# Performance work log

Measured on AMD Instinct MI355X. Metric: run time of the kernel, lower is better.

The kernel has to match this reference:

```python
import jax, jax.numpy as jnp
import numpy as np

B, N, D, L, NREPEAT = 32, 577, 384, 12, 4
H = 4 * D  # mlp hidden
EPS = 1e-6


def ln(x, w, b):
    mu = jnp.mean(x, axis=-1, keepdims=True)
    var = jnp.mean(jnp.square(x - mu), axis=-1, keepdims=True)
    return (x - mu) * jax.lax.rsqrt(var + EPS) * w + b


def setup_inputs() -> dict:
    key = jax.random.key(0)
    ks = jax.random.split(key, 16)
    s = 0.02
    return {
        "x": jax.random.normal(ks[0], (B, N, D), dtype=jnp.float32),
        "norm1_w": jnp.ones((L, D), jnp.float32),
        "norm1_b": jnp.zeros((L, D), jnp.float32),
        "qkv_w": jax.random.normal(ks[1], (L, 3 * D, D), jnp.float32) * s,
        "qkv_b": jnp.zeros((L, 3 * D), jnp.float32),
        "qn_w": jnp.ones((L, D), jnp.float32),
        "qn_b": jnp.zeros((L, D), jnp.float32),
        "kn_w": jnp.ones((L, D), jnp.float32),
        "kn_b": jnp.zeros((L, D), jnp.float32),
        "an_w": jnp.ones((L, D), jnp.float32),
        "an_b": jnp.zeros((L, D), jnp.float32),
        "proj_w": jax.random.normal(ks[2], (L, D, D), jnp.float32) * s,
        "proj_b": jnp.zeros((L, D), jnp.float32),
        "ls1": jnp.full((L, D), 1e-5, jnp.float32),
        "norm2_w": jnp.ones((L, D), jnp.float32),
        "norm2_b": jnp.zeros((L, D), jnp.float32),
        "fc1_w": jax.random.normal(ks[3], (L, H, D), jnp.float32) * s,
        "fc1_b": jnp.zeros((L, H), jnp.float32),
        "fc2_w": jax.random.normal(ks[4], (L, D, H), jnp.float32) * s,
        "fc2_b": jnp.zeros((L, D), jnp.float32),
        "ls2": jnp.full((L, D), 1e-5, jnp.float32),
    }


def _forward(x, norm1_w, norm1_b, qkv_w, qkv_b, qn_w, qn_b, kn_w, kn_b,
             an_w, an_b, proj_w, proj_b, ls1, norm2_w, norm2_b,
             fc1_w, fc1_b, fc2_w, fc2_b, ls2):
    scale = 1.0 / np.sqrt(D).astype(np.float32)
    x_prime = x
    history = []  # list of [B, 1, D] cls tokens, grows each repeat
    for _ in range(NREPEAT):
        new_cls = x[:, 0:1]
        x = jnp.concatenate([new_cls, x_prime[:, 1:]], axis=1)  # [B, N, D]
        mem = jnp.concatenate([x] + history, axis=1)            # [B, N+t, D]
        for l in range(L):
            res1 = x
            xn = ln(x, norm1_w[l], norm1_b[l])
            # manual qkv split: q from normed x, k/v from UNNORMED mem
            q = xn @ qkv_w[l, :D].T + qkv_b[l, :D]
            k = mem @ qkv_w[l, D:2 * D].T + qkv_b[l, D:2 * D]
            v = mem @ qkv_w[l, 2 * D:].T + qkv_b[l, 2 * D:]
            q = ln(q, qn_w[l], qn_b[l])
            k = ln(k, kn_w[l], kn_b[l])
            # single-head SDPA over full width D
            attn = jax.nn.softmax(jnp.einsum('bqd,bkd->bqk', q, k) * scale, axis=-1)
            prod = jnp.einsum('bqk,bkd->bqd', attn, v)
            prod = ln(prod, an_w[l], an_b[l])
            proj = prod @ proj_w[l].T + proj_b[l]
            x = proj * ls1[l] + res1
            res2 = x
            x2 = ln(x, norm2_w[l], norm2_b[l])
            h = jax.nn.gelu(x2 @ fc1_w[l].T + fc1_b[l], approximate=False)
            x1 = h @ fc2_w[l].T + fc2_b[l]
            x = x1 * ls2[l] + res2
        history.append(new_cls)
    return x


def reference(x, norm1_w, norm1_b, qkv_w, qkv_b, qn_w, qn_b, kn_w, kn_b,
              an_w, an_b, proj_w, proj_b, ls1, norm2_w, norm2_b,
              fc1_w, fc1_b, fc2_w, fc2_b, ls2):
    return _forward(x, norm1_w, norm1_b, qkv_w, qkv_b, qn_w, qn_b, kn_w, kn_b,
                    an_w, an_b, proj_w, proj_b, ls1, norm2_w, norm2_b,
                    fc1_w, fc1_b, fc2_w, fc2_b, ls2)
```

## Files before the change

### kernel.cpp

```cpp
#include <hip/hip_runtime.h>
#include <math.h>

#define BB 32
#define NN 577
#define DD 384
#define HD 1536
#define LL 12
#define MP 640
#define NRPT 4

typedef __attribute__((ext_vector_type(8))) short bf16x8;
typedef __attribute__((ext_vector_type(4))) float f32x4;

__device__ __forceinline__ unsigned short f2bf(float f){
  unsigned u = __builtin_bit_cast(unsigned, f);
  u += 0x7fffu + ((u >> 16) & 1u);
  return (unsigned short)(u >> 16);
}
__device__ __forceinline__ float bf2f(unsigned short s){
  unsigned u = ((unsigned)s) << 16;
  return __builtin_bit_cast(float, u);
}

__device__ __forceinline__ void async16(void* lds, const void* g){
  __builtin_amdgcn_global_load_lds(
      (const __attribute__((address_space(1))) unsigned int*)g,
      (__attribute__((address_space(3))) unsigned int*)lds, 16, 0, 0);
}

__global__ void prep_k(float* __restrict__ x, const float* __restrict__ xp,
                       float* __restrict__ cls_r, const float* __restrict__ cls_hist,
                       unsigned short* __restrict__ mem, int r){
  int i = blockIdx.x * 256 + threadIdx.x;
  if (i >= BB*MP*DD) return;
  int d = i % DD;
  int n = (i / DD) % MP;
  int b = i / (MP*DD);
  float v;
  if (n == 0){ v = x[(size_t)b*NN*DD + d]; cls_r[b*DD + d] = v; }
  else if (n < NN){ v = xp[((size_t)b*NN + n)*DD + d]; x[((size_t)b*NN + n)*DD + d] = v; }
  else if (n < NN + r){ v = cls_hist[(size_t)(n-NN)*BB*DD + b*DD + d]; }
  else v = 0.f;
  mem[i] = f2bf(v);
}

__global__ void cast_all_k(const float* __restrict__ qkvw, const float* __restrict__ pw,
                           const float* __restrict__ f1w, const float* __restrict__ f2w,
                           unsigned short* __restrict__ wbuf){
  int i = blockIdx.x * 256 + threadIdx.x;
  const int QKV = 3*DD*DD;
  const int PRJ = DD*DD;
  const int F1  = HD*DD;
  const int TOT = QKV + PRJ + 2*F1;
  if (i >= LL*TOT) return;
  int l = i / TOT, j = i % TOT;
  float v;
  if (j < QKV) v = qkvw[(size_t)l*QKV + j];
  else if (j < QKV+PRJ) v = pw[(size_t)l*PRJ + (j-QKV)];
  else if (j < QKV+PRJ+F1) v = f1w[(size_t)l*F1 + (j-QKV-PRJ)];
  else v = f2w[(size_t)l*F1 + (j-QKV-PRJ-F1)];
  wbuf[i] = f2bf(v);
}

template<typename T>
__global__ __launch_bounds__(256) void ln4_k(const T* __restrict__ in, const float* __restrict__ w,
                                             const float* __restrict__ bias, unsigned short* __restrict__ out,
                                             int nrows){
  int row = blockIdx.x*4 + (threadIdx.x >> 6);
  if (row >= nrows) return;
  int lane = threadIdx.x & 63;
  const T* p = in + (size_t)row*DD;
  float v[6];
  if constexpr (sizeof(T) == 4){
    const float* pf = (const float*)p;
    float4 a = *(const float4*)(pf + lane*4);
    float2 c = *(const float2*)(pf + 256 + lane*2);
    v[0]=a.x; v[1]=a.y; v[2]=a.z; v[3]=a.w; v[4]=c.x; v[5]=c.y;
  } else {
    const unsigned short* ps = (const unsigned short*)p;
    ushort4 a = *(const ushort4*)(ps + lane*4);
    ushort2 c = *(const ushort2*)(ps + 256 + lane*2);
    v[0]=bf2f(a.x); v[1]=bf2f(a.y); v[2]=bf2f(a.z); v[3]=bf2f(a.w);
    v[4]=bf2f(c.x); v[5]=bf2f(c.y);
  }
  float s = v[0]+v[1]+v[2]+v[3]+v[4]+v[5];
  #pragma unroll
  for (int o=32;o;o>>=1) s += __shfl_xor(s, o, 64);
  float mu = s * (1.f/DD);
  float q = 0.f;
  #pragma unroll
  for (int i=0;i<6;i++){ float t = v[i]-mu; q += t*t; }
  #pragma unroll
  for (int o=32;o;o>>=1) q += __shfl_xor(q, o, 64);
  float rs = rsqrtf(q*(1.f/DD) + 1e-6f);
  float4 w4 = *(const float4*)(w + lane*4);
  float2 w2 = *(const float2*)(w + 256 + lane*2);
  float4 b4 = *(const float4*)(bias + lane*4);
  float2 b2 = *(const float2*)(bias + 256 + lane*2);
  unsigned short* po = out + (size_t)row*DD;
  ushort4 o4;
  o4.x = f2bf((v[0]-mu)*rs*w4.x + b4.x);
  o4.y = f2bf((v[1]-mu)*rs*w4.y + b4.y);
  o4.z = f2bf((v[2]-mu)*rs*w4.z + b4.z);
  o4.w = f2bf((v[3]-mu)*rs*w4.w + b4.w);
  *(ushort4*)(po + lane*4) = o4;
  ushort2 o2;
  o2.x = f2bf((v[4]-mu)*rs*w2.x + b2.x);
  o2.y = f2bf((v[5]-mu)*rs*w2.y + b2.y);
  *(ushort2*)(po + 256 + lane*2) = o2;
}

__global__ __launch_bounds__(256) void fixup_k(
    const unsigned short* __restrict__ mem,
    const unsigned short* __restrict__ wq,
    const float* __restrict__ qkvb,
    const float* __restrict__ knw, const float* __restrict__ knb,
    unsigned short* __restrict__ kc,
    unsigned short* __restrict__ vc,
    int row2){
  int task = blockIdx.x*4 + (threadIdx.x >> 6);
  int lane = threadIdx.x & 63;
  int kind = task & 1;
  int rsel = (task >> 1) & 1;
  int b    = task >> 2;
  int row  = rsel ? row2 : 0;
  const unsigned short* mrow = mem + ((size_t)b*MP + row)*DD;
  const unsigned short* W = wq + (size_t)(kind+1)*DD*DD;
  const float* bias = qkvb + (kind+1)*DD;

  float acc[6] = {0,0,0,0,0,0};
  for (int i=0;i<48;i++){
    bf16x8 m8 = *(const bf16x8*)(mrow + i*8);
    float mf[8];
    #pragma unroll
    for (int j=0;j<8;j++) mf[j] = bf2f((unsigned short)m8[j]);
    #pragma unroll
    for (int c=0;c<6;c++){
      bf16x8 w8 = *(const bf16x8*)(W + (size_t)(lane + c*64)*DD + i*8);
      #pragma unroll
      for (int j=0;j<8;j++) acc[c] += mf[j]*bf2f((unsigned short)w8[j]);
    }
  }
  #pragma unroll
  for (int c=0;c<6;c++) acc[c] += bias[lane + c*64];

  if (kind == 0){
    float s1 = 0.f, s2 = 0.f;
    #pragma unroll
    for (int c=0;c<6;c++){ s1 += acc[c]; s2 += acc[c]*acc[c]; }
    #pragma unroll
    for (int o=32;o;o>>=1){ s1 += __shfl_xor(s1, o, 64); s2 += __shfl_xor(s2, o, 64); }
    float mu = s1*(1.f/DD);
    float var = s2*(1.f/DD) - mu*mu;
    float rs = rsqrtf(fmaxf(var, 0.f) + 1e-6f);
    unsigned short* out = kc + ((size_t)b*MP + row)*DD;
    #pragma unroll
    for (int c=0;c<6;c++){
      int col = lane + c*64;
      out[col] = f2bf((acc[c]-mu)*rs*knw[col] + knb[col]);
    }
  } else {
    #pragma unroll
    for (int c=0;c<6;c++){
      int d = lane + c*64;
      vc[((size_t)b*DD + d)*MP + row] = f2bf(acc[c]);
    }
  }
}

template<int EPI>
__global__ __launch_bounds__(256) void gemm128(
    const unsigned short* __restrict__ A, int lda, int arows, long sA,
    const unsigned short* __restrict__ B, int ldb, int brows, long sB,
    const float* __restrict__ bias,
    int K, int N,
    float* __restrict__ outF, unsigned short* __restrict__ outB,
    int ldo, int orows, long sO,
    const float* __restrict__ ls){

  __shared__ unsigned short a_sh[2][128*32];
  __shared__ unsigned short b_sh[2][128*32];

  int tid  = threadIdx.x;
  int wave = tid >> 6, lane = tid & 63;
  int lr = lane & 15, kg = lane >> 4;
  int wm = wave >> 1, wn = wave & 1;
  int z = blockIdx.z;
  int row0 = blockIdx.y * 128;
  int col0 = blockIdx.x * 128;

  const unsigned short* Ab = A + (size_t)z*sA;
  const unsigned short* Bb = B + (size_t)z*sB;

  f32x4 zf = {0.f,0.f,0.f,0.f};
  f32x4 acc[4][4];
  #pragma unroll
  for (int i=0;i<4;i++)
    #pragma unroll
    for (int j=0;j<4;j++) acc[i][j] = zf;

  int ra[2], rb[2], kc[2];
  #pragma unroll
  for (int it=0; it<2; it++){
    int c = tid + it*256;
    int r = row0 + (c>>2); if (r > arows-1) r = arows-1;
    ra[it] = r;
    r = col0 + (c>>2); if (r > brows-1) r = brows-1;
    rb[it] = r;
    kc[it] = (c&3)*8;
  }

  for (int k0 = 0; k0 < K; k0 += 64){
    #pragma unroll
    for (int p=0;p<2;p++){
      #pragma unroll
      for (int it=0; it<2; it++){
        unsigned short* la = &a_sh[p][(it*256 + wave*64)*8];
        unsigned short* lb = &b_sh[p][(it*256 + wave*64)*8];
        async16(la, Ab + (size_t)ra[it]*lda + k0 + p*32 + kc[it]);
        async16(lb, Bb + (size_t)rb[it]*ldb + k0 + p*32 + kc[it]);
      }
    }
    __syncthreads();
    #pragma unroll
    for (int p=0;p<2;p++){
      bf16x8 af[4], bfr[4];
      #pragma unroll
      for (int i=0;i<4;i++){
        af[i]  = *(const bf16x8*)&a_sh[p][(wm*64 + i*16 + lr)*32 + kg*8];
        bfr[i] = *(const bf16x8*)&b_sh[p][(wn*64 + i*16 + lr)*32 + kg*8];
      }
      #pragma unroll
      for (int i=0;i<4;i++)
        #pragma unroll
        for (int j=0;j<4;j++)
          acc[i][j] = __builtin_amdgcn_mfma_f32_16x16x32_bf16(af[i], bfr[j], acc[i][j], 0,0,0);
    }
    __syncthreads();
  }

  float* oF = outF ? outF + (size_t)z*sO : nullptr;
  unsigned short* oB = outB ? outB + (size_t)z*sO : nullptr;

  #pragma unroll
  for (int mi=0;mi<4;mi++)
    #pragma unroll
    for (int ni=0;ni<4;ni++)
      #pragma unroll
      for (int r=0;r<4;r++){
        int row = row0 + wm*64 + mi*16 + kg*4 + r;
        int col = col0 + wn*64 + ni*16 + lr;
        if (row >= orows || col >= N) continue;
        float vv = acc[mi][ni][r];
        size_t idx = (size_t)row*ldo + col;
        if (EPI == 0){
          if (bias) vv += bias[col];
          oB[idx] = f2bf(vv);
        } else if (EPI == 1){
          vv += bias[row];
          oB[idx] = f2bf(vv);
        } else if (EPI == 2){
          vv += bias[col];
          oF[idx] = vv*ls[col] + oF[idx];
        } else {
          vv += bias[col];
          float g = 0.5f*vv*(1.f + erff(vv*0.70710678118f));
          oB[idx] = f2bf(g);
        }
      }
}

__global__ __launch_bounds__(256, 2) void attn_k(
    const unsigned short* __restrict__ qraw,
    const float* __restrict__ qw, const float* __restrict__ qb_,
    const unsigned short* __restrict__ kb,
    const unsigned short* __restrict__ vT,
    const float* __restrict__ anw, const float* __restrict__ anb,
    unsigned short* __restrict__ out, int M){

  __shared__ unsigned short k_sh[32*384];
  __shared__ unsigned short v_sh[384*32];
  __shared__ unsigned short p_sh[64*56];

  int tid = threadIdx.x;
  int wv = tid >> 6, lane = tid & 63;
  int lr = lane & 15, kg = lane >> 4;
  int b = blockIdx.y, qt0 = blockIdx.x * 64;

  bf16x8 qf[12];
  {
    int qrow = qt0 + wv*16 + lr; if (qrow > NN-1) qrow = NN-1;
    const unsigned short* qp = qraw + ((size_t)b*NN + qrow)*DD;
    float s1 = 0.f, s2 = 0.f;
    #pragma unroll
    for (int ks=0; ks<12; ks++){
      qf[ks] = *(const bf16x8*)(qp + ks*32 + kg*8);
      #pragma unroll
      for (int j=0;j<8;j++){
        float t = bf2f((unsigned short)qf[ks][j]);
        s1 += t; s2 += t*t;
      }
    }
    s1 += __shfl_xor(s1, 16, 64); s1 += __shfl_xor(s1, 32, 64);
    s2 += __shfl_xor(s2, 16, 64); s2 += __shfl_xor(s2, 32, 64);
    const float SC = 0.05103103588f;
    float mu = s1 * (1.f/DD);
    float var = s2 * (1.f/DD) - mu*mu;
    float rs = rsqrtf(fmaxf(var, 0.f) + 1e-6f) * SC;
    #pragma unroll
    for (int ks=0; ks<12; ks++){
      int c0 = ks*32 + kg*8;
      float4 wa = *(const float4*)(qw + c0);
      float4 wb = *(const float4*)(qw + c0 + 4);
      float4 ba = *(const float4*)(qb_ + c0);
      float4 bb = *(const float4*)(qb_ + c0 + 4);
      bf16x8 t;
      t[0] = (short)f2bf((bf2f((unsigned short)qf[ks][0])-mu)*rs*wa.x + ba.x*SC);
      t[1] = (short)f2bf((bf2f((unsigned short)qf[ks][1])-mu)*rs*wa.y + ba.y*SC);
      t[2] = (short)f2bf((bf2f((unsigned short)qf[ks][2])-mu)*rs*wa.z + ba.z*SC);
      t[3] = (short)f2bf((bf2f((unsigned short)qf[ks][3])-mu)*rs*wa.w + ba.w*SC);
      t[4] = (short)f2bf((bf2f((unsigned short)qf[ks][4])-mu)*rs*wb.x + bb.x*SC);
      t[5] = (short)f2bf((bf2f((unsigned short)qf[ks][5])-mu)*rs*wb.y + bb.y*SC);
      t[6] = (short)f2bf((bf2f((unsigned short)qf[ks][6])-mu)*rs*wb.z + bb.z*SC);
      t[7] = (short)f2bf((bf2f((unsigned short)qf[ks][7])-mu)*rs*wb.w + bb.w*SC);
      qf[ks] = t;
    }
  }

  f32x4 zf = {0.f,0.f,0.f,0.f};
  f32x4 O[24];
  #pragma unroll
  for (int i=0;i<24;i++) O[i] = zf;
  float m_run[4], l_run[4];
  #pragma unroll
  for (int r=0;r<4;r++){ m_run[r] = -INFINITY; l_run[r] = 0.f; }

  for (int kt=0; kt<19; kt++){
    __syncthreads();
    #pragma unroll
    for (int i=0;i<6;i++){
      int L = i*256 + tid;
      int row = L/48, c = L%48;
      int gc = (c & ~7) | ((c ^ row) & 7);
      async16(&k_sh[L*8], kb + ((size_t)b*MP + kt*32 + row)*DD + gc*8);
    }
    #pragma unroll
    for (int i=0;i<6;i++){
      int L = i*256 + tid;
      int row = L>>2;
      int gc = (L&3) ^ (row&3);
      async16(&v_sh[L*8], vT + ((size_t)b*DD + row)*MP + kt*32 + gc*8);
    }
    __syncthreads();

    f32x4 s[2] = {zf, zf};
    __builtin_amdgcn_s_setprio(1);
    #pragma unroll
    for (int ks=0; ks<12; ks++){
      int c = ks*4 + kg;
      #pragma unroll
      for (int nk=0; nk<2; nk++){
        int krow = nk*16 + lr;
        bf16x8 bk = *(const bf16x8*)&k_sh[krow*DD + ((c & ~7) | ((c ^ krow)&7))*8];
        s[nk] = __builtin_amdgcn_mfma_f32_16x16x32_bf16(qf[ks], bk, s[nk], 0,0,0);
      }
    }
    __builtin_amdgcn_s_setprio(0);
    #pragma unroll
    for (int nk=0; nk<2; nk++){
      if (kt*32 + nk*16 + lr >= M){
        s[nk][0] = -INFINITY; s[nk][1] = -INFINITY; s[nk][2] = -INFINITY; s[nk][3] = -INFINITY;
      }
    }
    float vmax[4];
    #pragma unroll
    for (int r=0;r<4;r++){
      float v = fmaxf(s[0][r], s[1][r]);
      v = fmaxf(v, __shfl_xor(v, 1, 64));
      v = fmaxf(v, __shfl_xor(v, 2, 64));
      v = fmaxf(v, __shfl_xor(v, 4, 64));
      v = fmaxf(v, __shfl_xor(v, 8, 64));
      vmax[r] = v;
    }
    bool small = (vmax[0] <= m_run[0] + 8.f) & (vmax[1] <= m_run[1] + 8.f)
               & (vmax[2] <= m_run[2] + 8.f) & (vmax[3] <= m_run[3] + 8.f);
    if (!__all(small)){
      #pragma unroll
      for (int r=0;r<4;r++){
        float mn = fmaxf(m_run[r], vmax[r]);
        float al = __expf(m_run[r] - mn);
        m_run[r] = mn;
        l_run[r] *= al;
        #pragma unroll
        for (int ni=0;ni<24;ni++) O[ni][r] *= al;
      }
    }
    #pragma unroll
    for (int nk=0;nk<2;nk++)
      #pragma unroll
      for (int r=0;r<4;r++)
        s[nk][r] = __expf(s[nk][r] - m_run[r]);
    #pragma unroll
    for (int r=0;r<4;r++){
      float v = s[0][r] + s[1][r];
      v += __shfl_xor(v, 1, 64);
      v += __shfl_xor(v, 2, 64);
      v += __shfl_xor(v, 4, 64);
      v += __shfl_xor(v, 8, 64);
      l_run[r] += v;
    }
    #pragma unroll
    for (int nk=0;nk<2;nk++)
      #pragma unroll
      for (int r=0;r<4;r++)
        p_sh[(wv*16 + kg*4 + r)*56 + nk*16 + lr] = f2bf(s[nk][r]);
    __syncthreads();

    bf16x8 ap = *(const bf16x8*)&p_sh[(wv*16 + lr)*56 + kg*8];
    __builtin_amdgcn_s_setprio(1);
    #pragma unroll
    for (int ni=0;ni<24;ni++){
      int d = ni*16 + lr;
      bf16x8 bv = *(const bf16x8*)&v_sh[d*32 + ((kg ^ (d&3))*8)];
      O[ni] = __builtin_amdgcn_mfma_f32_16x16x32_bf16(ap, bv, O[ni], 0,0,0);
    }
    __builtin_amdgcn_s_setprio(0);
  }

  float inv[4];
  #pragma unroll
  for (int r=0;r<4;r++) inv[r] = 1.f / l_run[r];
  float s1[4] = {0,0,0,0}, s2[4] = {0,0,0,0};
  #pragma unroll
  for (int ni=0;ni<24;ni++)
    #pragma unroll
    for (int r=0;r<4;r++){
      float x = O[ni][r]*inv[r];
      O[ni][r] = x;
      s1[r] += x; s2[r] += x*x;
    }
  #pragma unroll
  for (int r=0;r<4;r++){
    #pragma unroll
    for (int o=1;o<16;o<<=1){ s1[r] += __shfl_xor(s1[r], o, 64); s2[r] += __shfl_xor(s2[r], o, 64); }
  }
  float mu[4], rs[4];
  #pragma unroll
  for (int r=0;r<4;r++){
    mu[r] = s1[r]*(1.f/DD);
    float var = s2[r]*(1.f/DD) - mu[r]*mu[r];
    rs[r] = rsqrtf(fmaxf(var, 0.f) + 1e-6f);
  }
  int rowb = qt0 + wv*16 + kg*4;
  #pragma unroll
  for (int ni=0;ni<24;ni++){
    int col = ni*16 + lr;
    float wc = anw[col], bc = anb[col];
    #pragma unroll
    for (int r=0;r<4;r++){
      int qrow = rowb + r;
      if (qrow < NN)
        out[((size_t)b*NN + qrow)*DD + col] = f2bf((O[ni][r]-mu[r])*rs[r]*wc + bc);
    }
  }
}


extern "C" void kernel_launch(void* const* d_in, const int* in_sizes, int n_in,
                              void* d_out, int out_size, void* d_ws, size_t ws_size,
                              hipStream_t stream){
  const float* x_in = (const float*)d_in[0];
  const float* n1w  = (const float*)d_in[1];
  const float* n1b  = (const float*)d_in[2];
  const float* qkvw = (const float*)d_in[3];
  const float* qkvb = (const float*)d_in[4];
  const float* qnw  = (const float*)d_in[5];
  const float* qnb  = (const float*)d_in[6];
  const float* knw  = (const float*)d_in[7];
  const float* knb  = (const float*)d_in[8];
  const float* anw  = (const float*)d_in[9];
  const float* anb  = (const float*)d_in[10];
  const float* pw   = (const float*)d_in[11];
  const float* pb   = (const float*)d_in[12];
  const float* ls1  = (const float*)d_in[13];
  const float* n2w  = (const float*)d_in[14];
  const float* n2b  = (const float*)d_in[15];
  const float* f1w  = (const float*)d_in[16];
  const float* f1b  = (const float*)d_in[17];
  const float* f2w  = (const float*)d_in[18];
  const float* f2bb = (const float*)d_in[19];
  const float* ls2  = (const float*)d_in[20];

  char* ws = (char*)d_ws;
  size_t off = 0;
  auto alloc = [&](size_t bytes)->char* {
    char* p = ws + off;
    off = (off + bytes + 255) & ~(size_t)255;
    return p;
  };

  const int QKV = 3*DD*DD, PRJ = DD*DD, F1 = HD*DD;
  const size_t WTOT = (size_t)QKV + PRJ + 2*F1;
  const size_t SLOT = (size_t)BB*MP*DD;

  unsigned short* wbuf  = (unsigned short*)alloc((size_t)LL*WTOT*2);
  float*          cls_h = (float*)         alloc((size_t)NRPT*BB*DD*4);
  unsigned short* mem_bf= (unsigned short*)alloc(SLOT*2);
  unsigned short* pool  = (unsigned short*)alloc(6*SLOT*2);
  unsigned short* kcache = (unsigned short*)alloc((size_t)LL*SLOT*2);
  unsigned short* vcache = (unsigned short*)alloc((size_t)LL*SLOT*2);
  bool use_cache = (off <= ws_size);

  unsigned short* S0 = pool;
  unsigned short* S1 = pool + SLOT;
  unsigned short* S2 = pool + 2*SLOT;
  unsigned short* S3 = pool + 3*SLOT;
  unsigned short* S5 = pool + 5*SLOT;

  unsigned short* xn    = S0;
  unsigned short* qraw  = S1;
  unsigned short* prodn = S3;
  unsigned short* x2    = S0;
  unsigned short* h     = S1;

  float* xf = (float*)d_out;

  auto cg = [](size_t n){ return dim3((unsigned)((n + 255) / 256)); };

  hipMemcpyAsync(xf, x_in, (size_t)BB*NN*DD*4, hipMemcpyDeviceToDevice, stream);

  const int RT  = (BB*NN + 127)/128;
  const int RTM = (BB*MP)/128;
  const int QR  = BB*NN;
  const int KR  = BB*MP;

  cast_all_k<<<cg((size_t)LL*WTOT),256,0,stream>>>(qkvw, pw, f1w, f2w, wbuf);

  for (int r = 0; r < NRPT; r++){
    int M = NN + r;
    prep_k<<<cg((size_t)BB*MP*DD),256,0,stream>>>(xf, x_in, cls_h + (size_t)r*BB*DD, cls_h, mem_bf, r);
    for (int l = 0; l < LL; l++){
      const unsigned short* wl = wbuf + (size_t)l*WTOT;
      const unsigned short* wq = wl;
      const unsigned short* wp = wl + QKV;
      const unsigned short* w1 = wl + QKV + PRJ;
      const unsigned short* w2 = wl + QKV + PRJ + F1;

      unsigned short* kbuf = use_cache ? kcache + (size_t)l*SLOT : S2;
      unsigned short* vbuf = use_cache ? vcache + (size_t)l*SLOT : S5;

      ln4_k<float><<<cg((size_t)QR*64),256,0,stream>>>(xf, n1w + l*DD, n1b + l*DD, xn, QR);
      gemm128<0><<<dim3(3,RT,1),256,0,stream>>>(xn,384,QR,0, wq,384,384,0,
          qkvb + l*3*DD, 384,384, nullptr,qraw,384,QR,0, nullptr);

      if (!use_cache || r == 0){
        gemm128<0><<<dim3(3,RTM,1),256,0,stream>>>(mem_bf,384,KR,0, wq + (size_t)DD*DD,384,384,0,
            qkvb + l*3*DD + DD, 384,384, nullptr,kbuf,384,KR,0, nullptr);
        gemm128<1><<<dim3(MP/128,3,BB),256,0,stream>>>(wq + (size_t)2*DD*DD,384,384,0, mem_bf,384,MP,(long)MP*DD,
            qkvb + l*3*DD + 2*DD, 384,MP, nullptr,vbuf,MP,384,(long)DD*MP, nullptr);
        ln4_k<unsigned short><<<cg((size_t)KR*64),256,0,stream>>>(kbuf, knw + l*DD, knb + l*DD, kbuf, KR);
      } else {
        fixup_k<<<32,256,0,stream>>>(mem_bf, wq, qkvb + l*3*DD,
                                     knw + l*DD, knb + l*DD, kbuf, vbuf, NN + r - 1);
      }

      attn_k<<<dim3(10,BB),256,0,stream>>>(qraw, qnw + l*DD, qnb + l*DD, kbuf, vbuf,
                                           anw + l*DD, anb + l*DD, prodn, M);
      gemm128<2><<<dim3(3,RT,1),256,0,stream>>>(prodn,384,QR,0, wp,384,384,0,
          pb + l*DD, 384,384, xf,nullptr,384,QR,0, ls1 + l*DD);
      ln4_k<float><<<cg((size_t)QR*64),256,0,stream>>>(xf, n2w + l*DD, n2b + l*DD, x2, QR);
      gemm128<3><<<dim3(HD/128,RT,1),256,0,stream>>>(x2,384,QR,0, w1,384,HD,0,
          f1b + l*HD, 384,HD, nullptr,h,HD,QR,0, nullptr);
      gemm128<2><<<dim3(3,RT,1),256,0,stream>>>(h,HD,QR,0, w2,HD,384,0,
          f2bb + l*DD, HD,384, xf,nullptr,384,QR,0, ls2 + l*DD);
    }
  }
}
```

Measured before the change: 16.55 ms.

## Shrink workspace pool and allow partial per-layer K/V caching across repeats

The workspace is re-laid out so activations share fewer slots: one bf16 slot plus a buffer sized for the MLP hidden activations. This frees room for K/V caches. When the full 12-layer cache does not fit, as many layers as possible are cached and the rest fall back to scratch buffers. Cached layers skip the full K/V projection on later repeats and use only a small fixup. prep_k also stops rewriting mem rows that do not change after the first repeat. This cuts redundant K/V GEMMs and memory writes, at the cost of extra buffer-aliasing logic whose benefit depends on the workspace size.

```diff
diff --git a/kernel.cpp b/kernel.cpp
--- a/kernel.cpp
+++ b/kernel.cpp
@@ -36,12 +36,12 @@
   int d = i % DD;
   int n = (i / DD) % MP;
   int b = i / (MP*DD);
-  float v;
+  float v; bool wr = true;
   if (n == 0){ v = x[(size_t)b*NN*DD + d]; cls_r[b*DD + d] = v; }
-  else if (n < NN){ v = xp[((size_t)b*NN + n)*DD + d]; x[((size_t)b*NN + n)*DD + d] = v; }
-  else if (n < NN + r){ v = cls_hist[(size_t)(n-NN)*BB*DD + b*DD + d]; }
-  else v = 0.f;
-  mem[i] = f2bf(v);
+  else if (n < NN){ v = xp[((size_t)b*NN + n)*DD + d]; x[((size_t)b*NN + n)*DD + d] = v; wr = (r==0); }
+  else if (n < NN + r){ v = cls_hist[(size_t)(n-NN)*BB*DD + b*DD + d]; wr = (n == NN + r - 1); }
+  else { v = 0.f; wr = (r==0); }
+  if (wr) mem[i] = f2bf(v);
 }
 
 __global__ void cast_all_k(const float* __restrict__ qkvw, const float* __restrict__ pw,
@@ -491,37 +491,48 @@
   const float* f2bb = (const float*)d_in[19];
   const float* ls2  = (const float*)d_in[20];
 
-  char* ws = (char*)d_ws;
-  size_t off = 0;
-  auto alloc = [&](size_t bytes)->char* {
-    char* p = ws + off;
-    off = (off + bytes + 255) & ~(size_t)255;
-    return p;
-  };
-
   const int QKV = 3*DD*DD, PRJ = DD*DD, F1 = HD*DD;
   const size_t WTOT = (size_t)QKV + PRJ + 2*F1;
   const size_t SLOT = (size_t)BB*MP*DD;
 
-  unsigned short* wbuf  = (unsigned short*)alloc((size_t)LL*WTOT*2);
-  float*          cls_h = (float*)         alloc((size_t)NRPT*BB*DD*4);
-  unsigned short* mem_bf= (unsigned short*)alloc(SLOT*2);
-  unsigned short* pool  = (unsigned short*)alloc(6*SLOT*2);
-  unsigned short* kcache = (unsigned short*)alloc((size_t)LL*SLOT*2);
-  unsigned short* vcache = (unsigned short*)alloc((size_t)LL*SLOT*2);
-  bool use_cache = (off <= ws_size);
-
-  unsigned short* S0 = pool;
-  unsigned short* S1 = pool + SLOT;
-  unsigned short* S2 = pool + 2*SLOT;
-  unsigned short* S3 = pool + 3*SLOT;
-  unsigned short* S5 = pool + 5*SLOT;
+  auto aln = [](size_t v){ return (v + 255) & ~(size_t)255; };
+  const size_t WB = aln(LL*WTOT*2);
+  const size_t CH = aln((size_t)NRPT*BB*DD*4);
+  const size_t MB_ = aln(SLOT*2);
+  const size_t SL = aln(SLOT*2);
+  const size_t HB = aln((size_t)BB*NN*HD*2);
+  const size_t CPL = 2*SL;
+
+  char* ws = (char*)d_ws;
+  size_t off = 0;
+  auto take = [&](size_t bytes)->char* { char* p = ws + off; off += bytes; return p; };
+
+  unsigned short* wbuf   = (unsigned short*)take(WB);
+  float*          cls_h  = (float*)         take(CH);
+  unsigned short* mem_bf = (unsigned short*)take(MB_);
+  unsigned short* S0     = (unsigned short*)take(SL);
+  unsigned short* HQ     = (unsigned short*)take(HB);
+
+  int nc;
+  unsigned short *kscr = nullptr, *vscr = nullptr, *kcache = nullptr, *vcache = nullptr;
+  if (off + (size_t)LL*CPL <= ws_size){
+    nc = LL;
+    kcache = (unsigned short*)take((size_t)LL*SL);
+    vcache = (unsigned short*)take((size_t)LL*SL);
+  } else {
+    kscr = (unsigned short*)take(SL);
+    vscr = (unsigned short*)take(SL);
+    size_t avail = (ws_size > off) ? ws_size - off : 0;
+    nc = (int)(avail / CPL); if (nc > LL) nc = LL; if (nc < 0) nc = 0;
+    kcache = (unsigned short*)take((size_t)nc*SL);
+    vcache = (unsigned short*)take((size_t)nc*SL);
+  }
 
   unsigned short* xn    = S0;
-  unsigned short* qraw  = S1;
-  unsigned short* prodn = S3;
+  unsigned short* qraw  = HQ;
+  unsigned short* prodn = S0;
   unsigned short* x2    = S0;
-  unsigned short* h     = S1;
+  unsigned short* h     = HQ;
 
   float* xf = (float*)d_out;
 
@@ -546,14 +557,15 @@
       const unsigned short* w1 = wl + QKV + PRJ;
       const unsigned short* w2 = wl + QKV + PRJ + F1;
 
-      unsigned short* kbuf = use_cache ? kcache + (size_t)l*SLOT : S2;
-      unsigned short* vbuf = use_cache ? vcache + (size_t)l*SLOT : S5;
+      bool cached = (l < nc);
+      unsigned short* kbuf = cached ? kcache + (size_t)l*SLOT : kscr;
+      unsigned short* vbuf = cached ? vcache + (size_t)l*SLOT : vscr;
 
       ln4_k<float><<<cg((size_t)QR*64),256,0,stream>>>(xf, n1w + l*DD, n1b + l*DD, xn, QR);
       gemm128<0><<<dim3(3,RT,1),256,0,stream>>>(xn,384,QR,0, wq,384,384,0,
           qkvb + l*3*DD, 384,384, nullptr,qraw,384,QR,0, nullptr);
 
-      if (!use_cache || r == 0){
+      if (!cached || r == 0){
         gemm128<0><<<dim3(3,RTM,1),256,0,stream>>>(mem_bf,384,KR,0, wq + (size_t)DD*DD,384,384,0,
             qkvb + l*3*DD + DD, 384,384, nullptr,kbuf,384,KR,0, nullptr);
         gemm128<1><<<dim3(MP/128,3,BB),256,0,stream>>>(wq + (size_t)2*DD*DD,384,384,0, mem_bf,384,MP,(long)MP*DD,
```

Measured after the change: 16.84 ms. Within noise of the previous version (+1.8%).
